# Optimization experiments

Hardware: AMD Instinct MI355X
Metric: run time of the kernel (lower is better)

The kernel has to match this reference:

```python
import jax, jax.numpy as jnp
import numpy as np


def _gcn_conv(x, W, b, src, dst, n_nodes):
    """PyG-style GCNConv: XW, symmetric deg^-1/2 normalization over edges
    (with self-loops already included in src/dst), scatter-add to targets, + bias."""
    xw = x @ W  # [N, F_out]
    ones = jnp.ones(src.shape[0], dtype=xw.dtype)
    deg = jax.ops.segment_sum(ones, dst, num_segments=n_nodes)  # in-degree incl. self-loops
    dinv = jnp.where(deg > 0, jax.lax.rsqrt(jnp.maximum(deg, 1.0)), 0.0)
    norm = dinv[src] * dinv[dst]                        # [E]
    msgs = xw[src] * norm[:, None]                      # [E, F_out] gather + scale
    out = jax.ops.segment_sum(msgs, dst, num_segments=n_nodes)  # scatter-add
    return out + b


def setup_inputs() -> dict:
    key = jax.random.key(0)
    k1, k2, k3, k4 = jax.random.split(key, 4)
    N, E = 100000, 1600000
    IN, HID, OUT = 128, 64, 64
    x = jax.random.normal(k1, (N, IN), dtype=jnp.float32)
    edge_index = jax.random.randint(k2, (2, E), 0, N, dtype=jnp.int64)
    W1 = jax.random.normal(k3, (IN, HID), dtype=jnp.float32) * (1.0 / np.sqrt(IN))
    b1 = jnp.zeros((HID,), dtype=jnp.float32)
    W2 = jax.random.normal(k4, (HID, OUT), dtype=jnp.float32) * (1.0 / np.sqrt(HID))
    b2 = jnp.zeros((OUT,), dtype=jnp.float32)
    return {"x": x, "edge_index": edge_index, "W1": W1, "b1": b1, "W2": W2, "b2": b2}


def reference(x, edge_index, W1, b1, W2, b2):
    n_nodes = x.shape[0]
    # add self-loops (PyG GCNConv default add_self_loops=True)
    loops = jnp.arange(n_nodes, dtype=edge_index.dtype)
    src = jnp.concatenate([edge_index[0], loops])
    dst = jnp.concatenate([edge_index[1], loops])
    h = _gcn_conv(x, W1, b1, src, dst, n_nodes)
    h = jax.nn.relu(h)
    z = _gcn_conv(h, W2, b2, src, dst, n_nodes)
    return z
```

## Files before the change

### kernel.cpp

```cpp
#include <hip/hip_runtime.h>

#define IN_F 128
#define HID_F 64
#define BKT_SHIFT 9
#define BKT_SIZE 512
#define CHUNK 4096

typedef unsigned short ushort_t;
typedef __attribute__((ext_vector_type(8))) short bf16x8;
typedef __attribute__((ext_vector_type(8))) unsigned short u16x8;
typedef __attribute__((ext_vector_type(4))) float f32x4;

__device__ inline ushort_t f2bf(float f) {
    unsigned u = __float_as_uint(f);
    u += 0x7FFFu + ((u >> 16) & 1u);
    return (ushort_t)(u >> 16);
}
__device__ inline float bf2f(ushort_t u) {
    return __uint_as_float((unsigned)u << 16);
}


__global__ __launch_bounds__(256) void k_hist_pack(const int* __restrict__ dst,
        int* __restrict__ ghist, int E, int nbE,
        const float* __restrict__ W1, const float* __restrict__ W2,
        ushort_t* __restrict__ Bp1, ushort_t* __restrict__ Bp2) {
    int tid = threadIdx.x;
    if ((int)blockIdx.x >= nbE) {
        int id = ((int)blockIdx.x - nbE) * 256 + tid;
        int iw = (id < 8192) ? id : id - 8192;
        int j = iw & 7, lane = (iw >> 3) & 63, t = (iw >> 9) & 3, s = iw >> 11;
        int k = s * 32 + ((lane >> 4) << 3) + j;
        int n = t * 16 + (lane & 15);
        if (id < 8192)        Bp1[iw] = f2bf(W1[k * 64 + n]);
        else if (id < 12288)  Bp2[iw] = f2bf(W2[k * 64 + n]);
        return;
    }
    __shared__ int hist[256];
    hist[tid] = 0;
    __syncthreads();
    int e0 = blockIdx.x * CHUNK, e1 = min(e0 + CHUNK, E);
    for (int e = e0 + tid; e < e1; e += 256)
        atomicAdd(&hist[dst[e] >> BKT_SHIFT], 1);
    __syncthreads();
    ghist[blockIdx.x * 256 + tid] = hist[tid];
}

__global__ __launch_bounds__(256) void k_colscan(int* __restrict__ ghist,
        int* __restrict__ gcount, int nb) {
    __shared__ int s[256];
    int t = threadIdx.x;
    int b = blockIdx.x;
    int j0 = 2 * t, j1 = 2 * t + 1;
    int v0 = (j0 < nb) ? ghist[j0 * 256 + b] : 0;
    int v1 = (j1 < nb) ? ghist[j1 * 256 + b] : 0;
    int p = v0 + v1;
    s[t] = p;
    __syncthreads();
    for (int off = 1; off < 256; off <<= 1) {
        int v = (t >= off) ? s[t - off] : 0;
        __syncthreads();
        s[t] += v;
        __syncthreads();
    }
    int excl = s[t] - p;
    if (j0 < nb) ghist[j0 * 256 + b] = excl;
    if (j1 < nb) ghist[j1 * 256 + b] = excl + v0;
    if (t == 255) gcount[b] = s[255];
}

__global__ __launch_bounds__(256) void k_bscan(const int* __restrict__ gcount,
        int* __restrict__ gbase, int* __restrict__ bbase,
        int* __restrict__ rowptr, int N, int E) {
    __shared__ int s[256];
    int t = threadIdx.x;
    int c = gcount[t];
    s[t] = c;
    __syncthreads();
    for (int off = 1; off < 256; off <<= 1) {
        int v = (t >= off) ? s[t - off] : 0;
        __syncthreads();
        s[t] += v;
        __syncthreads();
    }
    int base = s[t] - c;
    gbase[t] = base;
    bbase[t] = base;
    if (t == 255) bbase[256] = s[255];
    if (t == 0) rowptr[N] = E;
}

__global__ __launch_bounds__(256) void k_scatter(const int* __restrict__ src,
        const int* __restrict__ dst, const int* __restrict__ ghist,
        const int* __restrict__ gbase, unsigned* __restrict__ gbin, int E) {
    __shared__ int cur[256];
    int tid = threadIdx.x;
    cur[tid] = ghist[blockIdx.x * 256 + tid] + gbase[tid];
    __syncthreads();
    int e0 = blockIdx.x * CHUNK, e1 = min(e0 + CHUNK, E);
    for (int e = e0 + tid; e < e1; e += 256) {
        int d = dst[e];
        int b = d >> BKT_SHIFT;
        int p = atomicAdd(&cur[b], 1);
        gbin[p] = ((unsigned)(d & (BKT_SIZE - 1)) << 23) | (unsigned)src[e];
    }
}

__global__ __launch_bounds__(256) void k_fill2(const unsigned* __restrict__ gbin,
        const int* __restrict__ bbase, int* __restrict__ rowptr,
        float* __restrict__ dinv, int* __restrict__ col, int N) {
    __shared__ int cnt[BKT_SIZE];
    __shared__ int pos[BKT_SIZE];
    __shared__ int s[256];
    int tid = threadIdx.x;
    int b = blockIdx.x;
    int e0 = bbase[b], e1 = bbase[b + 1];
    cnt[tid] = 0; cnt[tid + 256] = 0;
    __syncthreads();
    for (int e = e0 + tid; e < e1; e += 256)
        atomicAdd(&cnt[gbin[e] >> 23], 1);
    __syncthreads();
    int c0 = cnt[2 * tid], c1 = cnt[2 * tid + 1];
    int p2 = c0 + c1;
    s[tid] = p2;
    __syncthreads();
    for (int off = 1; off < 256; off <<= 1) {
        int v = (tid >= off) ? s[tid - off] : 0;
        __syncthreads();
        s[tid] += v;
        __syncthreads();
    }
    int excl = s[tid] - p2;
    pos[2 * tid] = excl;
    pos[2 * tid + 1] = excl + c0;
    __syncthreads();
    int n0 = b << BKT_SHIFT;
    #pragma unroll
    for (int i = tid; i < BKT_SIZE; i += 256) {
        int n = n0 + i;
        if (n < N) {
            rowptr[n] = e0 + pos[i];
            dinv[n] = rsqrtf((float)cnt[i] + 1.0f);
        }
    }
    __syncthreads();
    for (int e = e0 + tid; e < e1; e += 256) {
        unsigned v = gbin[e];
        int p = atomicAdd(&pos[v >> 23], 1);
        col[e0 + p] = (int)(v & 0x7FFFFFu);
    }
}

template<int K, typename AT>
__global__ __launch_bounds__(256) void k_gemm_mfma(const AT* __restrict__ A,
        const ushort_t* __restrict__ Bp, const float* __restrict__ dinv,
        ushort_t* __restrict__ out, int N) {
    int wave = threadIdx.x >> 6, lane = threadIdx.x & 63;
    int m = lane & 15, q = lane >> 4;
    int row0 = blockIdx.x * 64 + wave * 16;
    int arow = row0 + m;
    int arowc = (arow < N) ? arow : (N - 1);
    f32x4 acc[4] = {};
    #pragma unroll
    for (int s = 0; s < K / 32; ++s) {
        bf16x8 af;
        if constexpr (sizeof(AT) == 4) {
            const float* ap = (const float*)A + (size_t)arowc * K + s * 32 + q * 8;
            float4 x0 = *(const float4*)ap;
            float4 x1 = *(const float4*)(ap + 4);
            af[0] = (short)f2bf(x0.x); af[1] = (short)f2bf(x0.y);
            af[2] = (short)f2bf(x0.z); af[3] = (short)f2bf(x0.w);
            af[4] = (short)f2bf(x1.x); af[5] = (short)f2bf(x1.y);
            af[6] = (short)f2bf(x1.z); af[7] = (short)f2bf(x1.w);
        } else {
            af = *(const bf16x8*)((const ushort_t*)A + (size_t)arowc * K + s * 32 + q * 8);
        }
        #pragma unroll
        for (int t = 0; t < 4; ++t) {
            bf16x8 bf = *(const bf16x8*)(Bp + (size_t)((s * 4 + t) * 64 + lane) * 8);
            acc[t] = __builtin_amdgcn_mfma_f32_16x16x32_bf16(af, bf, acc[t], 0, 0, 0);
        }
    }
    int orow0 = row0 + q * 4;
    float4 d4 = *(const float4*)(dinv + orow0);
    #pragma unroll
    for (int r = 0; r < 4; ++r) {
        int row = orow0 + r;
        if (row < N) {
            float dn = (r == 0) ? d4.x : (r == 1) ? d4.y : (r == 2) ? d4.z : d4.w;
            #pragma unroll
            for (int t = 0; t < 4; ++t)
                out[(size_t)row * 64 + t * 16 + m] = f2bf(acc[t][r] * dn);
        }
    }
}

__global__ __launch_bounds__(256) void k_aggregate(const ushort_t* __restrict__ xws,
        const int* __restrict__ rowptr, const int* __restrict__ col,
        const float* __restrict__ dinv, const float* __restrict__ bias,
        float* __restrict__ outf, ushort_t* __restrict__ outb, int N, int relu_bf16) {
    int n = (blockIdx.x * 256 + threadIdx.x) >> 3;
    int i = threadIdx.x & 7;
    if (n >= N) return;
    int beg = rowptr[n], end = rowptr[n + 1];
    float dn = dinv[n];
    const ushort_t* base = xws + i * 8;
    u16x8 sv = *(const u16x8*)(base + (size_t)n * 64);
    float a[8];
    #pragma unroll
    for (int k = 0; k < 8; ++k) a[k] = bf2f(sv[k]);
    int e = beg;
    for (; e + 8 <= end; e += 8) {
        int c[8];
        #pragma unroll
        for (int j = 0; j < 8; ++j) c[j] = col[e + j];
        u16x8 v[8];
        #pragma unroll
        for (int j = 0; j < 8; ++j) v[j] = *(const u16x8*)(base + (size_t)c[j] * 64);
        #pragma unroll
        for (int j = 0; j < 8; ++j)
            #pragma unroll
            for (int k = 0; k < 8; ++k) a[k] += bf2f(v[j][k]);
    }
    if (e + 4 <= end) {
        int c[4];
        #pragma unroll
        for (int j = 0; j < 4; ++j) c[j] = col[e + j];
        u16x8 v[4];
        #pragma unroll
        for (int j = 0; j < 4; ++j) v[j] = *(const u16x8*)(base + (size_t)c[j] * 64);
        #pragma unroll
        for (int j = 0; j < 4; ++j)
            #pragma unroll
            for (int k = 0; k < 8; ++k) a[k] += bf2f(v[j][k]);
        e += 4;
    }
    for (; e < end; ++e) {
        u16x8 v = *(const u16x8*)(base + (size_t)col[e] * 64);
        #pragma unroll
        for (int k = 0; k < 8; ++k) a[k] += bf2f(v[k]);
    }
    float4 b0 = *(const float4*)(bias + i * 8);
    float4 b1 = *(const float4*)(bias + i * 8 + 4);
    float r[8];
    r[0] = dn * a[0] + b0.x; r[1] = dn * a[1] + b0.y;
    r[2] = dn * a[2] + b0.z; r[3] = dn * a[3] + b0.w;
    r[4] = dn * a[4] + b1.x; r[5] = dn * a[5] + b1.y;
    r[6] = dn * a[6] + b1.z; r[7] = dn * a[7] + b1.w;
    if (relu_bf16) {
        u16x8 o;
        #pragma unroll
        for (int k = 0; k < 8; ++k) o[k] = f2bf(fmaxf(r[k], 0.f));
        *(u16x8*)(outb + (size_t)n * 64 + i * 8) = o;
    } else {
        float4 o0 = {r[0], r[1], r[2], r[3]};
        float4 o1 = {r[4], r[5], r[6], r[7]};
        *(float4*)(outf + (size_t)n * 64 + i * 8) = o0;
        *(float4*)(outf + (size_t)n * 64 + i * 8 + 4) = o1;
    }
}


extern "C" void kernel_launch(void* const* d_in, const int* in_sizes, int n_in,
                              void* d_out, int out_size, void* d_ws, size_t ws_size,
                              hipStream_t stream) {
    const float* x  = (const float*)d_in[0];
    const int*   ei = (const int*)d_in[1];
    const float* W1 = (const float*)d_in[2];
    const float* b1 = (const float*)d_in[3];
    const float* W2 = (const float*)d_in[4];
    const float* b2 = (const float*)d_in[5];
    float* out = (float*)d_out;

    const int N = in_sizes[0] / IN_F;
    const int E = in_sizes[1] / 2;
    const int* src = ei;
    const int* dst = ei + E;

    char* ws = (char*)d_ws;
    const size_t MB = 1u << 20;
    int*      bbase   = (int*)     (ws + 4096);
    int*      gbase   = (int*)     (ws + 8192);
    int*      gcount  = (int*)     (ws + 12288);
    ushort_t* Bp1     = (ushort_t*)(ws + 16384);
    ushort_t* Bp2     = (ushort_t*)(ws + 49152);
    int*      rowptr  = (int*)     (ws + 1 * MB);
    float*    dinv    = (float*)   (ws + 2 * MB);
    unsigned* gbin    = (unsigned*)(ws + 3 * MB);
    int*      ghist   = (int*)     (ws + 10 * MB);
    int*      col     = (int*)     (ws + 11 * MB);
    ushort_t* xws     = (ushort_t*)(ws + 20 * MB);
    ushort_t* h       = (ushort_t*)(ws + 36 * MB);

    const int nbE = (E + CHUNK - 1) / CHUNK;
    const int nbB = (N + BKT_SIZE - 1) / BKT_SIZE;
    const int nbG = (N + 63) / 64;
    const int nbA = (N * 8 + 255) / 256;

    k_hist_pack<<<nbE + 48, 256, 0, stream>>>(dst, ghist, E, nbE, W1, W2, Bp1, Bp2);
    k_colscan<<<256, 256, 0, stream>>>(ghist, gcount, nbE);
    k_bscan  <<<1, 256, 0, stream>>>(gcount, gbase, bbase, rowptr, N, E);
    k_scatter<<<nbE, 256, 0, stream>>>(src, dst, ghist, gbase, gbin, E);
    k_fill2  <<<nbB, 256, 0, stream>>>(gbin, bbase, rowptr, dinv, col, N);

    k_gemm_mfma<IN_F, float>   <<<nbG, 256, 0, stream>>>(x, Bp1, dinv, xws, N);
    k_aggregate<<<nbA, 256, 0, stream>>>(xws, rowptr, col, dinv, b1, nullptr, h, N, 1);

    k_gemm_mfma<HID_F, ushort_t><<<nbG, 256, 0, stream>>>(h, Bp2, dinv, xws, N);
    k_aggregate<<<nbA, 256, 0, stream>>>(xws, rowptr, col, dinv, b2, out, nullptr, N, 0);
}
```

Before: 231.6 us.

## Fuse layer-1 aggregation with layer-2 GEMM and fold bucket scan into consumers

The single-block k_bscan launch is removed. Each k_scatter and k_fill2 block now recomputes the 256-entry prefix scan of bucket counts in shared memory. The layer-1 aggregation now keeps 32 aggregated rows in LDS and runs the layer-2 MFMA GEMM on them directly, so the bf16 hidden activations are never written to or re-read from global memory and two launches are dropped. The cost is redundant scan work in every block, plus extra LDS use and a sync in the aggregation kernel, which may reduce occupancy.

```diff
diff --git a/kernel.cpp b/kernel.cpp
--- a/kernel.cpp
+++ b/kernel.cpp
@@ -69,33 +69,22 @@
     if (t == 255) gcount[b] = s[255];
 }
 
-__global__ __launch_bounds__(256) void k_bscan(const int* __restrict__ gcount,
-        int* __restrict__ gbase, int* __restrict__ bbase,
-        int* __restrict__ rowptr, int N, int E) {
-    __shared__ int s[256];
-    int t = threadIdx.x;
-    int c = gcount[t];
-    s[t] = c;
-    __syncthreads();
-    for (int off = 1; off < 256; off <<= 1) {
-        int v = (t >= off) ? s[t - off] : 0;
-        __syncthreads();
-        s[t] += v;
-        __syncthreads();
-    }
-    int base = s[t] - c;
-    gbase[t] = base;
-    bbase[t] = base;
-    if (t == 255) bbase[256] = s[255];
-    if (t == 0) rowptr[N] = E;
-}
-
 __global__ __launch_bounds__(256) void k_scatter(const int* __restrict__ src,
         const int* __restrict__ dst, const int* __restrict__ ghist,
-        const int* __restrict__ gbase, unsigned* __restrict__ gbin, int E) {
+        const int* __restrict__ gcount, unsigned* __restrict__ gbin, int E) {
     __shared__ int cur[256];
+    __shared__ int s[256];
     int tid = threadIdx.x;
-    cur[tid] = ghist[blockIdx.x * 256 + tid] + gbase[tid];
+    int gc = gcount[tid];
+    s[tid] = gc;
+    __syncthreads();
+    for (int off = 1; off < 256; off <<= 1) {
+        int v = (tid >= off) ? s[tid - off] : 0;
+        __syncthreads();
+        s[tid] += v;
+        __syncthreads();
+    }
+    cur[tid] = ghist[blockIdx.x * 256 + tid] + (s[tid] - gc);
     __syncthreads();
     int e0 = blockIdx.x * CHUNK, e1 = min(e0 + CHUNK, E);
     for (int e = e0 + tid; e < e1; e += 256) {
@@ -107,14 +96,26 @@
 }
 
 __global__ __launch_bounds__(256) void k_fill2(const unsigned* __restrict__ gbin,
-        const int* __restrict__ bbase, int* __restrict__ rowptr,
-        float* __restrict__ dinv, int* __restrict__ col, int N) {
+        const int* __restrict__ gcount, int* __restrict__ rowptr,
+        float* __restrict__ dinv, int* __restrict__ col, int N, int E) {
     __shared__ int cnt[BKT_SIZE];
     __shared__ int pos[BKT_SIZE];
     __shared__ int s[256];
     int tid = threadIdx.x;
     int b = blockIdx.x;
-    int e0 = bbase[b], e1 = bbase[b + 1];
+    int gc = gcount[tid];
+    s[tid] = gc;
+    __syncthreads();
+    for (int off = 1; off < 256; off <<= 1) {
+        int v = (tid >= off) ? s[tid - off] : 0;
+        __syncthreads();
+        s[tid] += v;
+        __syncthreads();
+    }
+    int e0 = (b > 0) ? s[b - 1] : 0;
+    int e1 = s[b];
+    if (b == 0 && tid == 0) rowptr[N] = E;
+    __syncthreads();
     cnt[tid] = 0; cnt[tid + 256] = 0;
     __syncthreads();
     for (int e = e0 + tid; e < e1; e += 256)
@@ -195,10 +196,100 @@
     }
 }
 
+__global__ __launch_bounds__(256) void k_agg_gemm(const ushort_t* __restrict__ xws,
+        const int* __restrict__ rowptr, const int* __restrict__ col,
+        const float* __restrict__ dinv, const float* __restrict__ bias,
+        const ushort_t* __restrict__ Bp2, ushort_t* __restrict__ out2, int N) {
+    __shared__ ushort_t hl[32][72];
+    int tid = threadIdx.x;
+    int nl = tid >> 3;
+    int i = tid & 7;
+    int n0 = blockIdx.x * 32;
+    int n = n0 + nl;
+    u16x8 hz = {};
+    if (n < N) {
+        int beg = rowptr[n], end = rowptr[n + 1];
+        float dn = dinv[n];
+        const ushort_t* base = xws + i * 8;
+        u16x8 sv = *(const u16x8*)(base + (size_t)n * 64);
+        float a[8];
+        #pragma unroll
+        for (int k = 0; k < 8; ++k) a[k] = bf2f(sv[k]);
+        int e = beg;
+        for (; e + 8 <= end; e += 8) {
+            int c[8];
+            #pragma unroll
+            for (int j = 0; j < 8; ++j) c[j] = col[e + j];
+            u16x8 v[8];
+            #pragma unroll
+            for (int j = 0; j < 8; ++j) v[j] = *(const u16x8*)(base + (size_t)c[j] * 64);
+            #pragma unroll
+            for (int j = 0; j < 8; ++j)
+                #pragma unroll
+                for (int k = 0; k < 8; ++k) a[k] += bf2f(v[j][k]);
+        }
+        if (e + 4 <= end) {
+            int c[4];
+            #pragma unroll
+            for (int j = 0; j < 4; ++j) c[j] = col[e + j];
+            u16x8 v[4];
+            #pragma unroll
+            for (int j = 0; j < 4; ++j) v[j] = *(const u16x8*)(base + (size_t)c[j] * 64);
+            #pragma unroll
+            for (int j = 0; j < 4; ++j)
+                #pragma unroll
+                for (int k = 0; k < 8; ++k) a[k] += bf2f(v[j][k]);
+            e += 4;
+        }
+        for (; e < end; ++e) {
+            u16x8 v = *(const u16x8*)(base + (size_t)col[e] * 64);
+            #pragma unroll
+            for (int k = 0; k < 8; ++k) a[k] += bf2f(v[k]);
+        }
+        float4 b0 = *(const float4*)(bias + i * 8);
+        float4 b1 = *(const float4*)(bias + i * 8 + 4);
+        float r[8];
+        r[0] = dn * a[0] + b0.x; r[1] = dn * a[1] + b0.y;
+        r[2] = dn * a[2] + b0.z; r[3] = dn * a[3] + b0.w;
+        r[4] = dn * a[4] + b1.x; r[5] = dn * a[5] + b1.y;
+        r[6] = dn * a[6] + b1.z; r[7] = dn * a[7] + b1.w;
+        #pragma unroll
+        for (int k = 0; k < 8; ++k) hz[k] = f2bf(fmaxf(r[k], 0.f));
+    }
+    *(u16x8*)&hl[nl][i * 8] = hz;
+    __syncthreads();
+    int w = tid >> 6, lane = tid & 63;
+    int m = lane & 15, q = lane >> 4;
+    int mt = w & 1;
+    int nt0 = (w >> 1) << 1;
+    f32x4 acc[2] = {};
+    #pragma unroll
+    for (int s = 0; s < 2; ++s) {
+        bf16x8 af = *(const bf16x8*)&hl[mt * 16 + m][s * 32 + q * 8];
+        #pragma unroll
+        for (int tt = 0; tt < 2; ++tt) {
+            bf16x8 bf = *(const bf16x8*)(Bp2 + (size_t)((s * 4 + nt0 + tt) * 64 + lane) * 8);
+            acc[tt] = __builtin_amdgcn_mfma_f32_16x16x32_bf16(af, bf, acc[tt], 0, 0, 0);
+        }
+    }
+    int orow0 = n0 + mt * 16 + q * 4;
+    float4 d4 = *(const float4*)(dinv + orow0);
+    #pragma unroll
+    for (int r = 0; r < 4; ++r) {
+        int row = orow0 + r;
+        if (row < N) {
+            float dn = (r == 0) ? d4.x : (r == 1) ? d4.y : (r == 2) ? d4.z : d4.w;
+            #pragma unroll
+            for (int tt = 0; tt < 2; ++tt)
+                out2[(size_t)row * 64 + (nt0 + tt) * 16 + m] = f2bf(acc[tt][r] * dn);
+        }
+    }
+}
+
 __global__ __launch_bounds__(256) void k_aggregate(const ushort_t* __restrict__ xws,
         const int* __restrict__ rowptr, const int* __restrict__ col,
         const float* __restrict__ dinv, const float* __restrict__ bias,
-        float* __restrict__ outf, ushort_t* __restrict__ outb, int N, int relu_bf16) {
+        float* __restrict__ outf, int N) {
     int n = (blockIdx.x * 256 + threadIdx.x) >> 3;
     int i = threadIdx.x & 7;
     if (n >= N) return;
@@ -242,22 +333,10 @@
     }
     float4 b0 = *(const float4*)(bias + i * 8);
     float4 b1 = *(const float4*)(bias + i * 8 + 4);
-    float r[8];
-    r[0] = dn * a[0] + b0.x; r[1] = dn * a[1] + b0.y;
-    r[2] = dn * a[2] + b0.z; r[3] = dn * a[3] + b0.w;
-    r[4] = dn * a[4] + b1.x; r[5] = dn * a[5] + b1.y;
-    r[6] = dn * a[6] + b1.z; r[7] = dn * a[7] + b1.w;
-    if (relu_bf16) {
-        u16x8 o;
-        #pragma unroll
-        for (int k = 0; k < 8; ++k) o[k] = f2bf(fmaxf(r[k], 0.f));
-        *(u16x8*)(outb + (size_t)n * 64 + i * 8) = o;
-    } else {
-        float4 o0 = {r[0], r[1], r[2], r[3]};
-        float4 o1 = {r[4], r[5], r[6], r[7]};
-        *(float4*)(outf + (size_t)n * 64 + i * 8) = o0;
-        *(float4*)(outf + (size_t)n * 64 + i * 8 + 4) = o1;
-    }
+    float4 o0 = {dn * a[0] + b0.x, dn * a[1] + b0.y, dn * a[2] + b0.z, dn * a[3] + b0.w};
+    float4 o1 = {dn * a[4] + b1.x, dn * a[5] + b1.y, dn * a[6] + b1.z, dn * a[7] + b1.w};
+    *(float4*)(outf + (size_t)n * 64 + i * 8) = o0;
+    *(float4*)(outf + (size_t)n * 64 + i * 8 + 4) = o1;
 }
 
 
@@ -279,8 +358,6 @@
 
     char* ws = (char*)d_ws;
     const size_t MB = 1u << 20;
-    int*      bbase   = (int*)     (ws + 4096);
-    int*      gbase   = (int*)     (ws + 8192);
     int*      gcount  = (int*)     (ws + 12288);
     ushort_t* Bp1     = (ushort_t*)(ws + 16384);
     ushort_t* Bp2     = (ushort_t*)(ws + 49152);
@@ -290,7 +367,7 @@
     int*      ghist   = (int*)     (ws + 10 * MB);
     int*      col     = (int*)     (ws + 11 * MB);
     ushort_t* xws     = (ushort_t*)(ws + 20 * MB);
-    ushort_t* h       = (ushort_t*)(ws + 36 * MB);
+    ushort_t* xws2    = (ushort_t*)(ws + 36 * MB);
 
     const int nbE = (E + CHUNK - 1) / CHUNK;
     const int nbB = (N + BKT_SIZE - 1) / BKT_SIZE;
@@ -299,13 +376,10 @@
 
     k_hist_pack<<<nbE + 48, 256, 0, stream>>>(dst, ghist, E, nbE, W1, W2, Bp1, Bp2);
     k_colscan<<<256, 256, 0, stream>>>(ghist, gcount, nbE);
-    k_bscan  <<<1, 256, 0, stream>>>(gcount, gbase, bbase, rowptr, N, E);
-    k_scatter<<<nbE, 256, 0, stream>>>(src, dst, ghist, gbase, gbin, E);
-    k_fill2  <<<nbB, 256, 0, stream>>>(gbin, bbase, rowptr, dinv, col, N);
-
-    k_gemm_mfma<IN_F, float>   <<<nbG, 256, 0, stream>>>(x, Bp1, dinv, xws, N);
-    k_aggregate<<<nbA, 256, 0, stream>>>(xws, rowptr, col, dinv, b1, nullptr, h, N, 1);
-
-    k_gemm_mfma<HID_F, ushort_t><<<nbG, 256, 0, stream>>>(h, Bp2, dinv, xws, N);
-    k_aggregate<<<nbA, 256, 0, stream>>>(xws, rowptr, col, dinv, b2, out, nullptr, N, 0);
-}
+    k_scatter<<<nbE, 256, 0, stream>>>(src, dst, ghist, gcount, gbin, E);
+    k_fill2  <<<nbB, 256, 0, stream>>>(gbin, gcount, rowptr, dinv, col, N, E);
+
+    k_gemm_mfma<IN_F, float><<<nbG, 256, 0, stream>>>(x, Bp1, dinv, xws, N);
+    k_agg_gemm<<<nbA, 256, 0, stream>>>(xws, rowptr, col, dinv, b1, Bp2, xws2, N);
+    k_aggregate<<<nbA, 256, 0, stream>>>(xws2, rowptr, col, dinv, b2, out, N);
+}
```

New measurement: 229.5 us. No clear change (-0.9%).
